# Optimization experiments

Measured on AMD Instinct MI355X. Metric: run time of the kernel, lower is better.

## Reference

```python
import jax, jax.numpy as jnp
import numpy as np

H = 256          # hidden_size
N_NODE = 50000   # item vocab
E_FULL = 500000  # full-graph edges
B = 1024         # sessions per batch
NODES_PER = 12   # session nodes per graph (contiguous, equal sections)
N = B * NODES_PER


def setup_inputs() -> dict:
    key = jax.random.key(0)
    ks = jax.random.split(key, 20)
    stdv = 1.0 / np.sqrt(H)
    u = lambda k, shape: jax.random.uniform(k, shape, jnp.float32, -stdv, stdv)
    return dict(
        x=jax.random.randint(ks[0], (N, 1), 1, N_NODE + 1, dtype=jnp.int32),  # 1-based item ids
        batch=jnp.repeat(jnp.arange(B, dtype=jnp.int32), NODES_PER),          # sorted graph ids
        edge_index=jax.random.randint(ks[1], (2, N), 0, N, dtype=jnp.int32),
        full_graph=jax.random.randint(ks[2], (2, E_FULL), 0, N_NODE, dtype=jnp.int32),
        emb=u(ks[3], (N_NODE, H)),
        ggnn_W=u(ks[4], (H, H)),
        gru_Wih=u(ks[5], (3 * H, H)),
        gru_Whh=u(ks[6], (3 * H, H)),
        gru_bih=u(ks[7], (3 * H,)),
        gru_bhh=u(ks[8], (3 * H,)),
        W1_w=u(ks[9], (H, H)), W1_b=u(ks[10], (H,)),
        W2_w=u(ks[11], (H, H)), W2_b=u(ks[12], (H,)),
        q_w=u(ks[13], (1, H)), q_b=u(ks[14], (1,)),
        W3_w=u(ks[15], (H, 2 * H)), W3_b=u(ks[16], (H,)),
    )


def _forward(x, batch, edge_index, full_graph, emb, ggnn_W, gru_Wih, gru_Whh,
             gru_bih, gru_bhh, W1_w, W1_b, W2_w, W2_b, q_w, q_b, W3_w, W3_b):
    # --- GatedGraphConv (num_layers=1) over the full item graph ---
    src, dst = full_graph[0], full_graph[1]
    m = emb @ ggnn_W                                      # [n_node, H]
    agg = jax.ops.segment_sum(m[src], dst, num_segments=N_NODE)  # sum aggregation
    # GRUCell(agg, emb)
    gi = agg @ gru_Wih.T + gru_bih                        # [n_node, 3H]
    gh = emb @ gru_Whh.T + gru_bhh
    i_r, i_z, i_n = jnp.split(gi, 3, axis=1)
    h_r, h_z, h_n = jnp.split(gh, 3, axis=1)
    r = jax.nn.sigmoid(i_r + h_r)
    z = jax.nn.sigmoid(i_z + h_z)
    n = jnp.tanh(i_n + r * h_n)
    hidden_all = (1.0 - z) * n + z * emb                  # [n_node, H]

    # gather session nodes (x is 1-based), relu
    h2 = jax.nn.relu(hidden_all[x[:, 0] - 1])             # [N, H]

    # --- Embedding2Score: segment attention readout ---
    sections = jax.ops.segment_sum(jnp.ones_like(batch), batch, num_segments=B)
    last_idx = jnp.cumsum(sections) - 1                   # last node of each session
    v_n = h2[last_idx]                                    # [B, H]
    v_n_rep = v_n[batch]                                  # [N, H]
    gate = jax.nn.sigmoid(v_n_rep @ W1_w.T + W1_b + h2 @ W2_w.T + W2_b)
    alpha = gate @ q_w.T + q_b                            # [N, 1]
    s_g = jax.ops.segment_sum(alpha * h2, batch, num_segments=B)  # [B, H]
    s_h = jnp.concatenate([v_n, s_g], axis=1) @ W3_w.T + W3_b     # [B, H]
    scores = s_h @ emb.T                                  # [B, n_node]
    return scores, h2


def reference(x, batch, edge_index, full_graph, emb, ggnn_W, gru_Wih, gru_Whh,
              gru_bih, gru_bhh, W1_w, W1_b, W2_w, W2_b, q_w, q_b, W3_w, W3_b):
    scores, h2 = _forward(x, batch, edge_index, full_graph, emb, ggnn_W,
                          gru_Wih, gru_Whh, gru_bih, gru_bhh,
                          W1_w, W1_b, W2_w, W2_b, q_w, q_b, W3_w, W3_b)
    return scores, h2, edge_index
```

## Files before the change

### kernel.cpp

```cpp
#include <hip/hip_runtime.h>
#include <hip/hip_bf16.h>
#include <stdint.h>

#define HDIM 256
#define NNODE 50000
#define EFULL 500000
#define BSESS 1024
#define NPER 12
#define NROWS 12288
#define CAP 96

typedef __attribute__((ext_vector_type(8))) short bf16x8;
typedef __attribute__((ext_vector_type(4))) float f32x4;
typedef __attribute__((ext_vector_type(4))) unsigned short u16x4;

__device__ __forceinline__ float bf2f(unsigned short v) {
  union { unsigned u; float f; } x; x.u = ((unsigned)v) << 16; return x.f;
}
__device__ __forceinline__ unsigned short f2bf(float f) {
  union { float f; unsigned u; } x; x.f = f;
  unsigned r = x.u + 0x7fff + ((x.u >> 16) & 1);
  return (unsigned short)(r >> 16);
}

__global__ void k_init_map(int* m, int* cnt) {
  int i = blockIdx.x * 256 + threadIdx.x;
  if (i < NNODE) m[i] = -1;
  if (i < NROWS) cnt[i] = 0;
}
__global__ void k_set_map(const int* __restrict__ x, int* __restrict__ m) {
  int i = blockIdx.x * 256 + threadIdx.x;
  if (i < NROWS) atomicMax(&m[x[i] - 1], i);
}

#define CV_EMB   12800000
#define CV_GW    65536
#define CV_WIH   196608
#define CV_WHH   196608
#define CV_W1    65536
#define CV_W2    65536
#define CV_W3    131072
#define CV_BIAS  2304
#define CV_TOTAL (CV_EMB + CV_GW + CV_WIH + CV_WHH + CV_W1 + CV_W2 + CV_W3 + CV_BIAS)
__global__ void k_conv(const float* __restrict__ emb, const float* __restrict__ gw,
                       const float* __restrict__ wih, const float* __restrict__ whh,
                       const float* __restrict__ w1, const float* __restrict__ w2,
                       const float* __restrict__ w3,
                       const float* __restrict__ bih, const float* __restrict__ bhh,
                       const float* __restrict__ w1b, const float* __restrict__ w2b,
                       const float* __restrict__ w3b,
                       unsigned short* __restrict__ embB, unsigned short* __restrict__ gwB,
                       unsigned short* __restrict__ wihB, unsigned short* __restrict__ whhB,
                       unsigned short* __restrict__ w1B, unsigned short* __restrict__ w2B,
                       unsigned short* __restrict__ w3B, unsigned short* __restrict__ biasB) {
  long idx = (long)blockIdx.x * 256 + threadIdx.x;
  if (idx < CV_EMB) { embB[idx] = f2bf(emb[idx]); return; }
  idx -= CV_EMB;
  if (idx < CV_GW)  { gwB[idx] = f2bf(gw[idx]); return; }
  idx -= CV_GW;
  if (idx < CV_WIH) { wihB[idx] = f2bf(wih[idx]); return; }
  idx -= CV_WIH;
  if (idx < CV_WHH) { whhB[idx] = f2bf(whh[idx]); return; }
  idx -= CV_WHH;
  if (idx < CV_W1)  { w1B[idx] = f2bf(w1[idx]); return; }
  idx -= CV_W1;
  if (idx < CV_W2)  { w2B[idx] = f2bf(w2[idx]); return; }
  idx -= CV_W2;
  if (idx < CV_W3)  { w3B[idx] = f2bf(w3[idx]); return; }
  idx -= CV_W3;
  if (idx < 768)        { biasB[idx] = f2bf(bih[idx]); return; }
  if (idx < 1536)       { biasB[idx] = f2bf(bhh[idx - 768]); return; }
  if (idx < 1792)       { biasB[idx] = f2bf(w1b[idx - 1536]); return; }
  if (idx < 2048)       { biasB[idx] = f2bf(w2b[idx - 1792]); return; }
  if (idx < CV_BIAS)    { biasB[idx] = f2bf(w3b[idx - 2048]); return; }
}

__global__ void k_bin(const int* __restrict__ fg, const int* __restrict__ map,
                      int* __restrict__ cnt, int* __restrict__ lists) {
  int e = blockIdx.x * 256 + threadIdx.x;
  if (e >= EFULL) return;
  int cid = map[fg[EFULL + e]];
  if (cid < 0) return;
  int pos = atomicAdd(&cnt[cid], 1);
  if (pos < CAP) lists[cid * CAP + pos] = fg[e];
}

__global__ __launch_bounds__(256) void k_aggsum(const int* __restrict__ cnt,
                                                const int* __restrict__ lists,
                                                const float* __restrict__ emb,
                                                unsigned short* __restrict__ Sb) {
  int i = blockIdx.x * 4 + (threadIdx.x >> 6);
  int lane = threadIdx.x & 63;
  int n = cnt[i];
  const int* lp = lists + (size_t)i * CAP;
  float sx = 0.f, sy = 0.f, sz = 0.f, sw = 0.f;
  int j = 0;
  for (; j + 4 <= n; j += 4) {
    int s0 = lp[j], s1 = lp[j + 1], s2 = lp[j + 2], s3 = lp[j + 3];
    float4 v0 = *(const float4*)(emb + (size_t)s0 * HDIM + lane * 4);
    float4 v1 = *(const float4*)(emb + (size_t)s1 * HDIM + lane * 4);
    float4 v2 = *(const float4*)(emb + (size_t)s2 * HDIM + lane * 4);
    float4 v3 = *(const float4*)(emb + (size_t)s3 * HDIM + lane * 4);
    sx += v0.x + v1.x + v2.x + v3.x;
    sy += v0.y + v1.y + v2.y + v3.y;
    sz += v0.z + v1.z + v2.z + v3.z;
    sw += v0.w + v1.w + v2.w + v3.w;
  }
  for (; j < n; j++) {
    int s0 = lp[j];
    float4 v0 = *(const float4*)(emb + (size_t)s0 * HDIM + lane * 4);
    sx += v0.x; sy += v0.y; sz += v0.z; sw += v0.w;
  }
  u16x4 o; o.x = f2bf(sx); o.y = f2bf(sy); o.z = f2bf(sz); o.w = f2bf(sw);
  *(u16x4*)(Sb + (size_t)i * HDIM + lane * 4) = o;
}

__global__ void k_bbig(const unsigned short* __restrict__ Pt, const unsigned short* __restrict__ Whh,
                       const float* __restrict__ bih, const float* __restrict__ bhh,
                       unsigned short* __restrict__ Bbig, unsigned short* __restrict__ biasBig) {
  int idx = blockIdx.x * 256 + threadIdx.x;
  if (idx < 1024 * 512) {
    int j = idx >> 9, c = idx & 511;
    unsigned short v = 0;
    if (c < 256) {
      if (j < 768) v = Pt[j * 256 + c];
    } else {
      int cc = c - 256;
      if (j < 512) v = Whh[j * 256 + cc];
      else if (j >= 768) v = Whh[(j - 256) * 256 + cc];
    }
    Bbig[idx] = v;
    return;
  }
  int jj = idx - 1024 * 512;
  if (jj < 512)       biasBig[jj] = f2bf(bih[jj] + bhh[jj]);
  else if (jj < 768)  biasBig[jj] = f2bf(bih[jj]);
  else if (jj < 1024) biasBig[jj] = f2bf(bhh[jj - 256]);
}

__global__ void k_gather(const int* __restrict__ x, const int* __restrict__ map,
                         const unsigned short* __restrict__ Sb, const float* __restrict__ emb,
                         unsigned short* __restrict__ Acat) {
  int i = blockIdx.x;
  int lane = threadIdx.x;
  int node = x[i] - 1;
  int cid = map[node];
  if (cid < 0) cid = 0;
  *(u16x4*)(Acat + (size_t)i * 512 + lane * 4) = *(const u16x4*)(Sb + (size_t)cid * HDIM + lane * 4);
  float4 v = *(const float4*)(emb + (size_t)node * HDIM + lane * 4);
  u16x4 o; o.x = f2bf(v.x); o.y = f2bf(v.y); o.z = f2bf(v.z); o.w = f2bf(v.w);
  *(u16x4*)(Acat + (size_t)i * 512 + 256 + lane * 4) = o;
}

__global__ void k_gru(const unsigned short* __restrict__ gall, const unsigned short* __restrict__ Acat,
                      unsigned short* __restrict__ h2b, float* __restrict__ h2out,
                      unsigned short* __restrict__ shin) {
  int idx = blockIdx.x * 256 + threadIdx.x;
  int row = idx >> 8, c = idx & 255;
  size_t base = (size_t)row * 1024;
  float rs = bf2f(gall[base + c]);
  float zs = bf2f(gall[base + 256 + c]);
  float inn = bf2f(gall[base + 512 + c]);
  float hn = bf2f(gall[base + 768 + c]);
  float r = 1.f / (1.f + expf(-rs));
  float z = 1.f / (1.f + expf(-zs));
  float n = tanhf(inn + r * hn);
  float e = bf2f(Acat[(size_t)row * 512 + 256 + c]);
  float h = fmaxf((1.f - z) * n + z * e, 0.f);
  unsigned short hb = f2bf(h);
  h2b[idx] = hb;
  h2out[idx] = h;
  if (row % NPER == NPER - 1) shin[(size_t)(row / NPER) * 512 + c] = hb;
}

__global__ void k_alpha(const unsigned short* __restrict__ t1, const unsigned short* __restrict__ t2,
                        const int* __restrict__ batch, const float* __restrict__ qw,
                        const float* __restrict__ qb, float* __restrict__ alpha) {
  int i = blockIdx.x, lane = threadIdx.x;
  int b = batch[i];
  u16x4 a = *(const u16x4*)(t1 + (size_t)b * HDIM + lane * 4);
  u16x4 c = *(const u16x4*)(t2 + (size_t)i * HDIM + lane * 4);
  float4 q = *(const float4*)(qw + lane * 4);
  float p = 0.f;
  p += q.x / (1.f + expf(-(bf2f(a.x) + bf2f(c.x))));
  p += q.y / (1.f + expf(-(bf2f(a.y) + bf2f(c.y))));
  p += q.z / (1.f + expf(-(bf2f(a.z) + bf2f(c.z))));
  p += q.w / (1.f + expf(-(bf2f(a.w) + bf2f(c.w))));
#pragma unroll
  for (int off = 32; off > 0; off >>= 1) p += __shfl_down(p, off);
  if (lane == 0) alpha[i] = p + qb[0];
}
__global__ void k_sg(const float* __restrict__ alpha, const unsigned short* __restrict__ h2b,
                     unsigned short* __restrict__ shin) {
  int b = blockIdx.x, c = threadIdx.x;
  float s = 0.f;
#pragma unroll
  for (int j = 0; j < NPER; j++)
    s += alpha[b * NPER + j] * bf2f(h2b[((size_t)b * NPER + j) * 256 + c]);
  shin[(size_t)b * 512 + 256 + c] = f2bf(s);
}
__global__ void k_edges(const int* __restrict__ e, float* __restrict__ out) {
  int i = blockIdx.x * 256 + threadIdx.x;
  if (i < 2 * NROWS) out[i] = (float)e[i];
}

template <bool OUT_BF16>
__global__ __launch_bounds__(256) void k_gemm_nt(
    const unsigned short* __restrict__ A, int lda,
    const unsigned short* __restrict__ Bm, int ldb,
    const unsigned short* __restrict__ bias,
    void* __restrict__ C, int ldc, int M, int N, int K) {
  __shared__ __align__(16) unsigned short As[128 * 32];
  __shared__ __align__(16) unsigned short Bs[128 * 32];
  const int tid = threadIdx.x;
  const int wid = tid >> 6, lane = tid & 63;
  const int quad = lane >> 4, l15 = lane & 15;
  const int m0 = blockIdx.x * 128, n0 = blockIdx.y * 128;
  const int wm = (wid & 1) * 64, wn = (wid >> 1) * 64;
  f32x4 acc[4][4] = {};
  const int lrow = tid >> 2;
  const int lcol = (tid & 3) * 8;
  const size_t ar0 = (size_t)min(m0 + lrow, M - 1) * lda + lcol;
  const size_t ar1 = (size_t)min(m0 + lrow + 64, M - 1) * lda + lcol;
  const size_t br0 = (size_t)min(n0 + lrow, N - 1) * ldb + lcol;
  const size_t br1 = (size_t)min(n0 + lrow + 64, N - 1) * ldb + lcol;
  const int ak = quad * 8;
  for (int k0 = 0; k0 < K; k0 += 32) {
    *(float4*)&As[(size_t)tid * 8]        = *(const float4*)&A[ar0 + k0];
    *(float4*)&As[2048 + (size_t)tid * 8] = *(const float4*)&A[ar1 + k0];
    *(float4*)&Bs[(size_t)tid * 8]        = *(const float4*)&Bm[br0 + k0];
    *(float4*)&Bs[2048 + (size_t)tid * 8] = *(const float4*)&Bm[br1 + k0];
    __syncthreads();
    bf16x8 af[4], bfv[4];
#pragma unroll
    for (int mi = 0; mi < 4; mi++) af[mi] = *(const bf16x8*)&As[(wm + mi * 16 + l15) * 32 + ak];
#pragma unroll
    for (int ni = 0; ni < 4; ni++) bfv[ni] = *(const bf16x8*)&Bs[(wn + ni * 16 + l15) * 32 + ak];
#pragma unroll
    for (int mi = 0; mi < 4; mi++)
#pragma unroll
      for (int ni = 0; ni < 4; ni++)
        acc[mi][ni] = __builtin_amdgcn_mfma_f32_16x16x32_bf16(af[mi], bfv[ni], acc[mi][ni], 0, 0, 0);
    __syncthreads();
  }
#pragma unroll
  for (int mi = 0; mi < 4; mi++) {
    const int gr0 = m0 + wm + mi * 16 + quad * 4;
#pragma unroll
    for (int ni = 0; ni < 4; ni++) {
      const int gc = n0 + wn + ni * 16 + l15;
      if (gc >= N) continue;
      const float bv = bias ? bf2f(bias[gc]) : 0.f;
#pragma unroll
      for (int r = 0; r < 4; r++) {
        const int gr = gr0 + r;
        if (gr < M) {
          const float v = acc[mi][ni][r] + bv;
          if (OUT_BF16) ((unsigned short*)C)[(size_t)gr * ldc + gc] = f2bf(v);
          else          ((float*)C)[(size_t)gr * ldc + gc] = v;
        }
      }
    }
  }
}

template <bool OUT_BF16>
__global__ __launch_bounds__(512) void k_gemm_nt2(
    const unsigned short* __restrict__ A, int lda,
    const unsigned short* __restrict__ Bm, int ldb,
    const unsigned short* __restrict__ bias,
    void* __restrict__ C, int ldc, int M, int N, int K) {
  __shared__ __align__(16) unsigned short As[256 * 32];
  __shared__ __align__(16) unsigned short Bs[128 * 32];
  const int tid = threadIdx.x;
  const int wid = tid >> 6, lane = tid & 63;
  const int quad = lane >> 4, l15 = lane & 15;
  const int m0 = blockIdx.x * 256, n0 = blockIdx.y * 128;
  const int wm = (wid & 3) * 64, wn = (wid >> 2) * 64;
  f32x4 acc[4][4] = {};
  const int lrow = tid >> 2;
  const int lcol = (tid & 3) * 8;
  const size_t ar0 = (size_t)min(m0 + lrow, M - 1) * lda + lcol;
  const size_t ar1 = (size_t)min(m0 + lrow + 128, M - 1) * lda + lcol;
  const size_t br0 = (size_t)min(n0 + lrow, N - 1) * ldb + lcol;
  const int ak = quad * 8;
  for (int k0 = 0; k0 < K; k0 += 32) {
    *(float4*)&As[(size_t)lrow * 32 + lcol]         = *(const float4*)&A[ar0 + k0];
    *(float4*)&As[(size_t)(lrow + 128) * 32 + lcol] = *(const float4*)&A[ar1 + k0];
    *(float4*)&Bs[(size_t)lrow * 32 + lcol]         = *(const float4*)&Bm[br0 + k0];
    __syncthreads();
    bf16x8 af[4], bfv[4];
#pragma unroll
    for (int mi = 0; mi < 4; mi++) af[mi] = *(const bf16x8*)&As[(wm + mi * 16 + l15) * 32 + ak];
#pragma unroll
    for (int ni = 0; ni < 4; ni++) bfv[ni] = *(const bf16x8*)&Bs[(wn + ni * 16 + l15) * 32 + ak];
#pragma unroll
    for (int mi = 0; mi < 4; mi++)
#pragma unroll
      for (int ni = 0; ni < 4; ni++)
        acc[mi][ni] = __builtin_amdgcn_mfma_f32_16x16x32_bf16(af[mi], bfv[ni], acc[mi][ni], 0, 0, 0);
    __syncthreads();
  }
#pragma unroll
  for (int mi = 0; mi < 4; mi++) {
    const int gr0 = m0 + wm + mi * 16 + quad * 4;
#pragma unroll
    for (int ni = 0; ni < 4; ni++) {
      const int gc = n0 + wn + ni * 16 + l15;
      if (gc >= N) continue;
      const float bv = bias ? bf2f(bias[gc]) : 0.f;
#pragma unroll
      for (int r = 0; r < 4; r++) {
        const int gr = gr0 + r;
        if (gr < M) {
          const float v = acc[mi][ni][r] + bv;
          if (OUT_BF16) ((unsigned short*)C)[(size_t)gr * ldc + gc] = f2bf(v);
          else          ((float*)C)[(size_t)gr * ldc + gc] = v;
        }
      }
    }
  }
}

extern "C" void kernel_launch(void* const* d_in, const int* in_sizes, int n_in,
                              void* d_out, int out_size, void* d_ws, size_t ws_size,
                              hipStream_t stream) {
  const int* x     = (const int*)d_in[0];
  const int* batch = (const int*)d_in[1];
  const int* eidx  = (const int*)d_in[2];
  const int* fg    = (const int*)d_in[3];
  const float* emb   = (const float*)d_in[4];
  const float* ggnnW = (const float*)d_in[5];
  const float* Wih   = (const float*)d_in[6];
  const float* Whh   = (const float*)d_in[7];
  const float* bih   = (const float*)d_in[8];
  const float* bhh   = (const float*)d_in[9];
  const float* W1w   = (const float*)d_in[10];
  const float* W1b   = (const float*)d_in[11];
  const float* W2w   = (const float*)d_in[12];
  const float* W2b   = (const float*)d_in[13];
  const float* qw    = (const float*)d_in[14];
  const float* qb    = (const float*)d_in[15];
  const float* W3w   = (const float*)d_in[16];
  const float* W3b   = (const float*)d_in[17];

  char* w = (char*)d_ws;
  size_t off = 0;
  auto alloc = [&](size_t bytes) { char* p = w + off; off += (bytes + 511) & ~(size_t)511; return p; };
  int*            map   = (int*)alloc((size_t)NNODE * 4);
  int*            cnt   = (int*)alloc((size_t)NROWS * 4);
  int*            lists = (int*)alloc((size_t)NROWS * CAP * 4);
  unsigned short* Sb    = (unsigned short*)alloc((size_t)NROWS * HDIM * 2);
  unsigned short* Acat  = (unsigned short*)alloc((size_t)NROWS * 512 * 2);
  unsigned short* gallC = (unsigned short*)alloc((size_t)NROWS * 1024 * 2);
  unsigned short* embB  = (unsigned short*)alloc((size_t)NNODE * HDIM * 2);
  unsigned short* gwB   = (unsigned short*)alloc((size_t)CV_GW * 2);
  unsigned short* WihB  = (unsigned short*)alloc((size_t)CV_WIH * 2);
  unsigned short* WhhB  = (unsigned short*)alloc((size_t)CV_WHH * 2);
  unsigned short* W1wB  = (unsigned short*)alloc((size_t)CV_W1 * 2);
  unsigned short* W2wB  = (unsigned short*)alloc((size_t)CV_W2 * 2);
  unsigned short* W3wB  = (unsigned short*)alloc((size_t)CV_W3 * 2);
  unsigned short* biasB = (unsigned short*)alloc((size_t)CV_BIAS * 2);
  unsigned short* Pt    = (unsigned short*)alloc((size_t)768 * 256 * 2);
  unsigned short* Bbig  = (unsigned short*)alloc((size_t)1024 * 512 * 2);
  unsigned short* biasBig = (unsigned short*)alloc((size_t)1024 * 2);
  unsigned short* h2b   = (unsigned short*)alloc((size_t)NROWS * HDIM * 2);
  unsigned short* t1    = (unsigned short*)alloc((size_t)BSESS * HDIM * 2);
  unsigned short* t2    = (unsigned short*)alloc((size_t)NROWS * HDIM * 2);
  float*          alpha = (float*)alloc((size_t)NROWS * 4);
  unsigned short* shin  = (unsigned short*)alloc((size_t)BSESS * 512 * 2);
  unsigned short* shb   = (unsigned short*)alloc((size_t)BSESS * HDIM * 2);
  if (off > ws_size) return;

  float* out_scores = (float*)d_out;
  float* out_h2     = out_scores + (size_t)BSESS * NNODE;
  float* out_e      = out_h2 + (size_t)NROWS * HDIM;

  dim3 blk(256);
  k_init_map<<<(NNODE + 255) / 256, blk, 0, stream>>>(map, cnt);
  k_set_map <<<(NROWS + 255) / 256, blk, 0, stream>>>(x, map);
  k_conv    <<<(CV_TOTAL + 255) / 256, blk, 0, stream>>>(emb, ggnnW, Wih, Whh, W1w, W2w, W3w,
                bih, bhh, W1b, W2b, W3b, embB, gwB, WihB, WhhB, W1wB, W2wB, W3wB, biasB);
  k_bin     <<<(EFULL + 255) / 256, blk, 0, stream>>>(fg, map, cnt, lists);
  k_aggsum  <<<NROWS / 4, blk, 0, stream>>>(cnt, lists, emb, Sb);
  k_gemm_nt<true><<<dim3(6, 2), blk, 0, stream>>>(WihB, HDIM, gwB, HDIM, nullptr, Pt, HDIM, 768, HDIM, HDIM);
  k_bbig    <<<(1024 * 512 + 1024 + 255) / 256, blk, 0, stream>>>(Pt, WhhB, bih, bhh, Bbig, biasBig);
  k_gather  <<<NROWS, 64, 0, stream>>>(x, map, Sb, emb, Acat);
  k_gemm_nt2<true><<<dim3(48, 8), dim3(512), 0, stream>>>(Acat, 512, Bbig, 512, biasBig, gallC, 1024, NROWS, 1024, 512);
  k_gru     <<<NROWS, blk, 0, stream>>>(gallC, Acat, h2b, out_h2, shin);
  k_gemm_nt<true><<<dim3(8, 2), blk, 0, stream>>>(shin, 512, W1wB, HDIM, biasB + 1536, t1, HDIM, BSESS, HDIM, HDIM);
  k_gemm_nt<true><<<dim3(96, 2), blk, 0, stream>>>(h2b, HDIM, W2wB, HDIM, biasB + 1792, t2, HDIM, NROWS, HDIM, HDIM);
  k_alpha   <<<NROWS, 64, 0, stream>>>(t1, t2, batch, qw, qb, alpha);
  k_sg      <<<BSESS, blk, 0, stream>>>(alpha, h2b, shin);
  k_gemm_nt<true><<<dim3(8, 2), blk, 0, stream>>>(shin, 512, W3wB, 512, biasB + 2048, shb, HDIM, BSESS, HDIM, 512);
  k_gemm_nt2<false><<<dim3(4, 391), dim3(512), 0, stream>>>(shb, HDIM, embB, HDIM, nullptr, out_scores, NNODE, BSESS, NNODE, HDIM);
  k_edges   <<<(2 * NROWS + 255) / 256, blk, 0, stream>>>(eidx, out_e);
}
```

Baseline: 511.6 us.

## Fuse GRU gates into GEMM epilogue and merge small pipeline kernels

Reorders the combined weight matrix so that each 64-column wave tile holds the r, z, n-input and n-hidden gates for the same 16 channels. The GRU nonlinearity can then run directly in the GEMM epilogue, which removes the 12288x1024 bf16 gate intermediate and the separate GRU kernel. Map and count initialisation and the edge copy move into the conversion kernel, and the aggregation kernel writes Acat directly, dropping the gather kernel and the Sb buffer. The t1 and t2 GEMMs share one launch, and the alpha and s_g kernels merge into one per-session attention kernel. The result is fewer launches and less intermediate traffic, with more complex index logic in exchange.

```diff
diff --git a/kernel.cpp b/kernel.cpp
--- a/kernel.cpp
+++ b/kernel.cpp
@@ -21,16 +21,6 @@
   union { float f; unsigned u; } x; x.f = f;
   unsigned r = x.u + 0x7fff + ((x.u >> 16) & 1);
   return (unsigned short)(r >> 16);
-}
-
-__global__ void k_init_map(int* m, int* cnt) {
-  int i = blockIdx.x * 256 + threadIdx.x;
-  if (i < NNODE) m[i] = -1;
-  if (i < NROWS) cnt[i] = 0;
-}
-__global__ void k_set_map(const int* __restrict__ x, int* __restrict__ m) {
-  int i = blockIdx.x * 256 + threadIdx.x;
-  if (i < NROWS) atomicMax(&m[x[i] - 1], i);
 }
 
 #define CV_EMB   12800000
@@ -41,7 +31,8 @@
 #define CV_W2    65536
 #define CV_W3    131072
 #define CV_BIAS  2304
-#define CV_TOTAL (CV_EMB + CV_GW + CV_WIH + CV_WHH + CV_W1 + CV_W2 + CV_W3 + CV_BIAS)
+#define CV_WSUM  (CV_EMB + CV_GW + CV_WIH + CV_WHH + CV_W1 + CV_W2 + CV_W3 + CV_BIAS)
+#define CV_TOTAL (CV_WSUM + NNODE + NROWS + 2 * NROWS)
 __global__ void k_conv(const float* __restrict__ emb, const float* __restrict__ gw,
                        const float* __restrict__ wih, const float* __restrict__ whh,
                        const float* __restrict__ w1, const float* __restrict__ w2,
@@ -52,7 +43,9 @@
                        unsigned short* __restrict__ embB, unsigned short* __restrict__ gwB,
                        unsigned short* __restrict__ wihB, unsigned short* __restrict__ whhB,
                        unsigned short* __restrict__ w1B, unsigned short* __restrict__ w2B,
-                       unsigned short* __restrict__ w3B, unsigned short* __restrict__ biasB) {
+                       unsigned short* __restrict__ w3B, unsigned short* __restrict__ biasB,
+                       int* __restrict__ map, int* __restrict__ cnt,
+                       const int* __restrict__ eidx, float* __restrict__ out_e) {
   long idx = (long)blockIdx.x * 256 + threadIdx.x;
   if (idx < CV_EMB) { embB[idx] = f2bf(emb[idx]); return; }
   idx -= CV_EMB;
@@ -68,11 +61,24 @@
   idx -= CV_W2;
   if (idx < CV_W3)  { w3B[idx] = f2bf(w3[idx]); return; }
   idx -= CV_W3;
-  if (idx < 768)        { biasB[idx] = f2bf(bih[idx]); return; }
-  if (idx < 1536)       { biasB[idx] = f2bf(bhh[idx - 768]); return; }
-  if (idx < 1792)       { biasB[idx] = f2bf(w1b[idx - 1536]); return; }
-  if (idx < 2048)       { biasB[idx] = f2bf(w2b[idx - 1792]); return; }
-  if (idx < CV_BIAS)    { biasB[idx] = f2bf(w3b[idx - 2048]); return; }
+  if (idx < CV_BIAS) {
+    if (idx < 768)        { biasB[idx] = f2bf(bih[idx]); return; }
+    if (idx < 1536)       { biasB[idx] = f2bf(bhh[idx - 768]); return; }
+    if (idx < 1792)       { biasB[idx] = f2bf(w1b[idx - 1536]); return; }
+    if (idx < 2048)       { biasB[idx] = f2bf(w2b[idx - 1792]); return; }
+    biasB[idx] = f2bf(w3b[idx - 2048]); return;
+  }
+  idx -= CV_BIAS;
+  if (idx < NNODE) { map[idx] = -1; return; }
+  idx -= NNODE;
+  if (idx < NROWS) { cnt[idx] = 0; return; }
+  idx -= NROWS;
+  if (idx < 2 * NROWS) out_e[idx] = (float)eidx[idx];
+}
+
+__global__ void k_set_map(const int* __restrict__ x, int* __restrict__ m) {
+  int i = blockIdx.x * 256 + threadIdx.x;
+  if (i < NROWS) atomicMax(&m[x[i] - 1], i);
 }
 
 __global__ void k_bin(const int* __restrict__ fg, const int* __restrict__ map,
@@ -85,14 +91,18 @@
   if (pos < CAP) lists[cid * CAP + pos] = fg[e];
 }
 
-__global__ __launch_bounds__(256) void k_aggsum(const int* __restrict__ cnt,
+__global__ __launch_bounds__(256) void k_aggsum(const int* __restrict__ x,
+                                                const int* __restrict__ map,
+                                                const int* __restrict__ cnt,
                                                 const int* __restrict__ lists,
                                                 const float* __restrict__ emb,
-                                                unsigned short* __restrict__ Sb) {
+                                                unsigned short* __restrict__ Acat) {
   int i = blockIdx.x * 4 + (threadIdx.x >> 6);
   int lane = threadIdx.x & 63;
-  int n = cnt[i];
-  const int* lp = lists + (size_t)i * CAP;
+  int node = x[i] - 1;
+  int cid = map[node];
+  int n = cnt[cid];
+  const int* lp = lists + (size_t)cid * CAP;
   float sx = 0.f, sy = 0.f, sz = 0.f, sw = 0.f;
   int j = 0;
   for (; j + 4 <= n; j += 4) {
@@ -112,110 +122,54 @@
     sx += v0.x; sy += v0.y; sz += v0.z; sw += v0.w;
   }
   u16x4 o; o.x = f2bf(sx); o.y = f2bf(sy); o.z = f2bf(sz); o.w = f2bf(sw);
-  *(u16x4*)(Sb + (size_t)i * HDIM + lane * 4) = o;
+  *(u16x4*)(Acat + (size_t)i * 512 + lane * 4) = o;
+  float4 v = *(const float4*)(emb + (size_t)node * HDIM + lane * 4);
+  u16x4 o2; o2.x = f2bf(v.x); o2.y = f2bf(v.y); o2.z = f2bf(v.z); o2.w = f2bf(v.w);
+  *(u16x4*)(Acat + (size_t)i * 512 + 256 + lane * 4) = o2;
 }
 
 __global__ void k_bbig(const unsigned short* __restrict__ Pt, const unsigned short* __restrict__ Whh,
                        const float* __restrict__ bih, const float* __restrict__ bhh,
-                       unsigned short* __restrict__ Bbig, unsigned short* __restrict__ biasBig) {
+                       unsigned short* __restrict__ Bbig2, unsigned short* __restrict__ bias2) {
   int idx = blockIdx.x * 256 + threadIdx.x;
   if (idx < 1024 * 512) {
-    int j = idx >> 9, c = idx & 511;
+    int jp = idx >> 9, k = idx & 511;
+    int q = jp >> 6, g = (jp >> 4) & 3, t = jp & 15;
+    int c = q * 16 + t;
     unsigned short v = 0;
-    if (c < 256) {
-      if (j < 768) v = Pt[j * 256 + c];
+    if (k < 256) {
+      if (g < 3) v = Pt[(g * 256 + c) * 256 + k];
     } else {
-      int cc = c - 256;
-      if (j < 512) v = Whh[j * 256 + cc];
-      else if (j >= 768) v = Whh[(j - 256) * 256 + cc];
+      int kk = k - 256;
+      if (g < 2) v = Whh[(g * 256 + c) * 256 + kk];
+      else if (g == 3) v = Whh[(512 + c) * 256 + kk];
     }
-    Bbig[idx] = v;
+    Bbig2[idx] = v;
     return;
   }
-  int jj = idx - 1024 * 512;
-  if (jj < 512)       biasBig[jj] = f2bf(bih[jj] + bhh[jj]);
-  else if (jj < 768)  biasBig[jj] = f2bf(bih[jj]);
-  else if (jj < 1024) biasBig[jj] = f2bf(bhh[jj - 256]);
-}
-
-__global__ void k_gather(const int* __restrict__ x, const int* __restrict__ map,
-                         const unsigned short* __restrict__ Sb, const float* __restrict__ emb,
-                         unsigned short* __restrict__ Acat) {
-  int i = blockIdx.x;
-  int lane = threadIdx.x;
-  int node = x[i] - 1;
-  int cid = map[node];
-  if (cid < 0) cid = 0;
-  *(u16x4*)(Acat + (size_t)i * 512 + lane * 4) = *(const u16x4*)(Sb + (size_t)cid * HDIM + lane * 4);
-  float4 v = *(const float4*)(emb + (size_t)node * HDIM + lane * 4);
-  u16x4 o; o.x = f2bf(v.x); o.y = f2bf(v.y); o.z = f2bf(v.z); o.w = f2bf(v.w);
-  *(u16x4*)(Acat + (size_t)i * 512 + 256 + lane * 4) = o;
-}
-
-__global__ void k_gru(const unsigned short* __restrict__ gall, const unsigned short* __restrict__ Acat,
-                      unsigned short* __restrict__ h2b, float* __restrict__ h2out,
-                      unsigned short* __restrict__ shin) {
-  int idx = blockIdx.x * 256 + threadIdx.x;
-  int row = idx >> 8, c = idx & 255;
-  size_t base = (size_t)row * 1024;
-  float rs = bf2f(gall[base + c]);
-  float zs = bf2f(gall[base + 256 + c]);
-  float inn = bf2f(gall[base + 512 + c]);
-  float hn = bf2f(gall[base + 768 + c]);
-  float r = 1.f / (1.f + expf(-rs));
-  float z = 1.f / (1.f + expf(-zs));
-  float n = tanhf(inn + r * hn);
-  float e = bf2f(Acat[(size_t)row * 512 + 256 + c]);
-  float h = fmaxf((1.f - z) * n + z * e, 0.f);
-  unsigned short hb = f2bf(h);
-  h2b[idx] = hb;
-  h2out[idx] = h;
-  if (row % NPER == NPER - 1) shin[(size_t)(row / NPER) * 512 + c] = hb;
-}
-
-__global__ void k_alpha(const unsigned short* __restrict__ t1, const unsigned short* __restrict__ t2,
-                        const int* __restrict__ batch, const float* __restrict__ qw,
-                        const float* __restrict__ qb, float* __restrict__ alpha) {
-  int i = blockIdx.x, lane = threadIdx.x;
-  int b = batch[i];
-  u16x4 a = *(const u16x4*)(t1 + (size_t)b * HDIM + lane * 4);
-  u16x4 c = *(const u16x4*)(t2 + (size_t)i * HDIM + lane * 4);
-  float4 q = *(const float4*)(qw + lane * 4);
-  float p = 0.f;
-  p += q.x / (1.f + expf(-(bf2f(a.x) + bf2f(c.x))));
-  p += q.y / (1.f + expf(-(bf2f(a.y) + bf2f(c.y))));
-  p += q.z / (1.f + expf(-(bf2f(a.z) + bf2f(c.z))));
-  p += q.w / (1.f + expf(-(bf2f(a.w) + bf2f(c.w))));
-#pragma unroll
-  for (int off = 32; off > 0; off >>= 1) p += __shfl_down(p, off);
-  if (lane == 0) alpha[i] = p + qb[0];
-}
-__global__ void k_sg(const float* __restrict__ alpha, const unsigned short* __restrict__ h2b,
-                     unsigned short* __restrict__ shin) {
-  int b = blockIdx.x, c = threadIdx.x;
-  float s = 0.f;
-#pragma unroll
-  for (int j = 0; j < NPER; j++)
-    s += alpha[b * NPER + j] * bf2f(h2b[((size_t)b * NPER + j) * 256 + c]);
-  shin[(size_t)b * 512 + 256 + c] = f2bf(s);
-}
-__global__ void k_edges(const int* __restrict__ e, float* __restrict__ out) {
-  int i = blockIdx.x * 256 + threadIdx.x;
-  if (i < 2 * NROWS) out[i] = (float)e[i];
+  int jp = idx - 1024 * 512;
+  if (jp < 1024) {
+    int q = jp >> 6, g = (jp >> 4) & 3, t = jp & 15;
+    int c = q * 16 + t;
+    float bv;
+    if (g < 2)      bv = bih[g * 256 + c] + bhh[g * 256 + c];
+    else if (g == 2) bv = bih[512 + c];
+    else             bv = bhh[512 + c];
+    bias2[jp] = f2bf(bv);
+  }
 }
 
 template <bool OUT_BF16>
-__global__ __launch_bounds__(256) void k_gemm_nt(
+__device__ __forceinline__ void gemm128_body(
+    unsigned short* As, unsigned short* Bs,
     const unsigned short* __restrict__ A, int lda,
     const unsigned short* __restrict__ Bm, int ldb,
     const unsigned short* __restrict__ bias,
-    void* __restrict__ C, int ldc, int M, int N, int K) {
-  __shared__ __align__(16) unsigned short As[128 * 32];
-  __shared__ __align__(16) unsigned short Bs[128 * 32];
+    void* __restrict__ C, int ldc, int M, int N, int K, int bx, int by) {
   const int tid = threadIdx.x;
   const int wid = tid >> 6, lane = tid & 63;
   const int quad = lane >> 4, l15 = lane & 15;
-  const int m0 = blockIdx.x * 128, n0 = blockIdx.y * 128;
+  const int m0 = bx * 128, n0 = by * 128;
   const int wm = (wid & 1) * 64, wn = (wid >> 1) * 64;
   f32x4 acc[4][4] = {};
   const int lrow = tid >> 2;
@@ -262,6 +216,128 @@
       }
     }
   }
+}
+
+template <bool OUT_BF16>
+__global__ __launch_bounds__(256) void k_gemm_nt(
+    const unsigned short* __restrict__ A, int lda,
+    const unsigned short* __restrict__ Bm, int ldb,
+    const unsigned short* __restrict__ bias,
+    void* __restrict__ C, int ldc, int M, int N, int K) {
+  __shared__ __align__(16) unsigned short As[128 * 32];
+  __shared__ __align__(16) unsigned short Bs[128 * 32];
+  gemm128_body<OUT_BF16>(As, Bs, A, lda, Bm, ldb, bias, C, ldc, M, N, K, blockIdx.x, blockIdx.y);
+}
+
+__global__ __launch_bounds__(256) void k_t12(
+    const unsigned short* __restrict__ h2b, const unsigned short* __restrict__ W2, const unsigned short* __restrict__ b2,
+    unsigned short* __restrict__ t2,
+    const unsigned short* __restrict__ shin, const unsigned short* __restrict__ W1, const unsigned short* __restrict__ b1,
+    unsigned short* __restrict__ t1) {
+  __shared__ __align__(16) unsigned short As[128 * 32];
+  __shared__ __align__(16) unsigned short Bs[128 * 32];
+  if (blockIdx.x < 96)
+    gemm128_body<true>(As, Bs, h2b, HDIM, W2, HDIM, b2, t2, HDIM, NROWS, HDIM, HDIM, blockIdx.x, blockIdx.y);
+  else
+    gemm128_body<true>(As, Bs, shin, 512, W1, HDIM, b1, t1, HDIM, BSESS, HDIM, HDIM, blockIdx.x - 96, blockIdx.y);
+}
+
+__global__ __launch_bounds__(512) void k_ggru(
+    const unsigned short* __restrict__ Acat,
+    const unsigned short* __restrict__ Bbig2,
+    const unsigned short* __restrict__ bias2,
+    unsigned short* __restrict__ h2b, float* __restrict__ h2out,
+    unsigned short* __restrict__ shin) {
+  __shared__ __align__(16) unsigned short As[256 * 32];
+  __shared__ __align__(16) unsigned short Bs[128 * 32];
+  const int tid = threadIdx.x;
+  const int wid = tid >> 6, lane = tid & 63;
+  const int quad = lane >> 4, l15 = lane & 15;
+  const int m0 = blockIdx.x * 256, n0 = blockIdx.y * 128;
+  const int wm = (wid & 3) * 64, wn = (wid >> 2) * 64;
+  f32x4 acc[4][4] = {};
+  const int lrow = tid >> 2;
+  const int lcol = (tid & 3) * 8;
+  const size_t ar0 = (size_t)(m0 + lrow) * 512 + lcol;
+  const size_t ar1 = (size_t)(m0 + lrow + 128) * 512 + lcol;
+  const size_t br0 = (size_t)(n0 + lrow) * 512 + lcol;
+  const int ak = quad * 8;
+  for (int k0 = 0; k0 < 512; k0 += 32) {
+    *(float4*)&As[(size_t)lrow * 32 + lcol]         = *(const float4*)&Acat[ar0 + k0];
+    *(float4*)&As[(size_t)(lrow + 128) * 32 + lcol] = *(const float4*)&Acat[ar1 + k0];
+    *(float4*)&Bs[(size_t)lrow * 32 + lcol]         = *(const float4*)&Bbig2[br0 + k0];
+    __syncthreads();
+    bf16x8 af[4], bfv[4];
+#pragma unroll
+    for (int mi = 0; mi < 4; mi++) af[mi] = *(const bf16x8*)&As[(wm + mi * 16 + l15) * 32 + ak];
+#pragma unroll
+    for (int g = 0; g < 4; g++) bfv[g] = *(const bf16x8*)&Bs[(wn + g * 16 + l15) * 32 + ak];
+#pragma unroll
+    for (int mi = 0; mi < 4; mi++)
+#pragma unroll
+      for (int g = 0; g < 4; g++)
+        acc[mi][g] = __builtin_amdgcn_mfma_f32_16x16x32_bf16(af[mi], bfv[g], acc[mi][g], 0, 0, 0);
+    __syncthreads();
+  }
+  const int ch = ((n0 + wn) >> 2) + l15;
+  const float b0 = bf2f(bias2[(n0 + wn) + 0 * 16 + l15]);
+  const float b1 = bf2f(bias2[(n0 + wn) + 1 * 16 + l15]);
+  const float b2 = bf2f(bias2[(n0 + wn) + 2 * 16 + l15]);
+  const float b3 = bf2f(bias2[(n0 + wn) + 3 * 16 + l15]);
+#pragma unroll
+  for (int mi = 0; mi < 4; mi++) {
+    const int gr0 = m0 + wm + mi * 16 + quad * 4;
+#pragma unroll
+    for (int r = 0; r < 4; r++) {
+      const int gr = gr0 + r;
+      float rs = acc[mi][0][r] + b0;
+      float zs = acc[mi][1][r] + b1;
+      float inn = acc[mi][2][r] + b2;
+      float hn = acc[mi][3][r] + b3;
+      float rr = 1.f / (1.f + expf(-rs));
+      float zz = 1.f / (1.f + expf(-zs));
+      float nn = tanhf(inn + rr * hn);
+      float e = bf2f(Acat[(size_t)gr * 512 + 256 + ch]);
+      float h = fmaxf((1.f - zz) * nn + zz * e, 0.f);
+      unsigned short hb = f2bf(h);
+      h2b[(size_t)gr * HDIM + ch] = hb;
+      h2out[(size_t)gr * HDIM + ch] = h;
+      if (gr % NPER == NPER - 1) shin[(size_t)(gr / NPER) * 512 + ch] = hb;
+    }
+  }
+}
+
+__global__ __launch_bounds__(256) void k_attn(
+    const unsigned short* __restrict__ t1, const unsigned short* __restrict__ t2,
+    const unsigned short* __restrict__ h2b,
+    const float* __restrict__ qw, const float* __restrict__ qb,
+    unsigned short* __restrict__ shin) {
+  __shared__ float al[NPER];
+  const int b = blockIdx.x;
+  const int w = threadIdx.x >> 6, lane = threadIdx.x & 63;
+  u16x4 a = *(const u16x4*)(t1 + (size_t)b * HDIM + lane * 4);
+  float4 q = *(const float4*)(qw + lane * 4);
+  float ax = bf2f(a.x), ay = bf2f(a.y), az = bf2f(a.z), aw = bf2f(a.w);
+#pragma unroll
+  for (int i = 0; i < 3; i++) {
+    int j = w * 3 + i;
+    u16x4 c = *(const u16x4*)(t2 + ((size_t)b * NPER + j) * HDIM + lane * 4);
+    float p = 0.f;
+    p += q.x / (1.f + expf(-(ax + bf2f(c.x))));
+    p += q.y / (1.f + expf(-(ay + bf2f(c.y))));
+    p += q.z / (1.f + expf(-(az + bf2f(c.z))));
+    p += q.w / (1.f + expf(-(aw + bf2f(c.w))));
+#pragma unroll
+    for (int off = 32; off > 0; off >>= 1) p += __shfl_down(p, off);
+    if (lane == 0) al[j] = p + qb[0];
+  }
+  __syncthreads();
+  const int c = threadIdx.x;
+  float s = 0.f;
+#pragma unroll
+  for (int j = 0; j < NPER; j++)
+    s += al[j] * bf2f(h2b[((size_t)b * NPER + j) * HDIM + c]);
+  shin[(size_t)b * 512 + 256 + c] = f2bf(s);
 }
 
 template <bool OUT_BF16>
@@ -343,6 +419,7 @@
   const float* qb    = (const float*)d_in[15];
   const float* W3w   = (const float*)d_in[16];
   const float* W3b   = (const float*)d_in[17];
+  (void)batch;
 
   char* w = (char*)d_ws;
   size_t off = 0;
@@ -350,9 +427,7 @@
   int*            map   = (int*)alloc((size_t)NNODE * 4);
   int*            cnt   = (int*)alloc((size_t)NROWS * 4);
   int*            lists = (int*)alloc((size_t)NROWS * CAP * 4);
-  unsigned short* Sb    = (unsigned short*)alloc((size_t)NROWS * HDIM * 2);
   unsigned short* Acat  = (unsigned short*)alloc((size_t)NROWS * 512 * 2);
-  unsigned short* gallC = (unsigned short*)alloc((size_t)NROWS * 1024 * 2);
   unsigned short* embB  = (unsigned short*)alloc((size_t)NNODE * HDIM * 2);
   unsigned short* gwB   = (unsigned short*)alloc((size_t)CV_GW * 2);
   unsigned short* WihB  = (unsigned short*)alloc((size_t)CV_WIH * 2);
@@ -362,12 +437,11 @@
   unsigned short* W3wB  = (unsigned short*)alloc((size_t)CV_W3 * 2);
   unsigned short* biasB = (unsigned short*)alloc((size_t)CV_BIAS * 2);
   unsigned short* Pt    = (unsigned short*)alloc((size_t)768 * 256 * 2);
-  unsigned short* Bbig  = (unsigned short*)alloc((size_t)1024 * 512 * 2);
-  unsigned short* biasBig = (unsigned short*)alloc((size_t)1024 * 2);
+  unsigned short* Bbig2 = (unsigned short*)alloc((size_t)1024 * 512 * 2);
+  unsigned short* bias2 = (unsigned short*)alloc((size_t)1024 * 2);
   unsigned short* h2b   = (unsigned short*)alloc((size_t)NROWS * HDIM * 2);
   unsigned short* t1    = (unsigned short*)alloc((size_t)BSESS * HDIM * 2);
   unsigned short* t2    = (unsigned short*)alloc((size_t)NROWS * HDIM * 2);
-  float*          alpha = (float*)alloc((size_t)NROWS * 4);
   unsigned short* shin  = (unsigned short*)alloc((size_t)BSESS * 512 * 2);
   unsigned short* shb   = (unsigned short*)alloc((size_t)BSESS * HDIM * 2);
   if (off > ws_size) return;
@@ -377,22 +451,17 @@
   float* out_e      = out_h2 + (size_t)NROWS * HDIM;
 
   dim3 blk(256);
-  k_init_map<<<(NNODE + 255) / 256, blk, 0, stream>>>(map, cnt);
-  k_set_map <<<(NROWS + 255) / 256, blk, 0, stream>>>(x, map);
-  k_conv    <<<(CV_TOTAL + 255) / 256, blk, 0, stream>>>(emb, ggnnW, Wih, Whh, W1w, W2w, W3w,
-                bih, bhh, W1b, W2b, W3b, embB, gwB, WihB, WhhB, W1wB, W2wB, W3wB, biasB);
-  k_bin     <<<(EFULL + 255) / 256, blk, 0, stream>>>(fg, map, cnt, lists);
-  k_aggsum  <<<NROWS / 4, blk, 0, stream>>>(cnt, lists, emb, Sb);
+  k_conv   <<<(CV_TOTAL + 255) / 256, blk, 0, stream>>>(emb, ggnnW, Wih, Whh, W1w, W2w, W3w,
+               bih, bhh, W1b, W2b, W3b, embB, gwB, WihB, WhhB, W1wB, W2wB, W3wB, biasB,
+               map, cnt, eidx, out_e);
+  k_set_map<<<(NROWS + 255) / 256, blk, 0, stream>>>(x, map);
+  k_bin    <<<(EFULL + 255) / 256, blk, 0, stream>>>(fg, map, cnt, lists);
   k_gemm_nt<true><<<dim3(6, 2), blk, 0, stream>>>(WihB, HDIM, gwB, HDIM, nullptr, Pt, HDIM, 768, HDIM, HDIM);
-  k_bbig    <<<(1024 * 512 + 1024 + 255) / 256, blk, 0, stream>>>(Pt, WhhB, bih, bhh, Bbig, biasBig);
-  k_gather  <<<NROWS, 64, 0, stream>>>(x, map, Sb, emb, Acat);
-  k_gemm_nt2<true><<<dim3(48, 8), dim3(512), 0, stream>>>(Acat, 512, Bbig, 512, biasBig, gallC, 1024, NROWS, 1024, 512);
-  k_gru     <<<NROWS, blk, 0, stream>>>(gallC, Acat, h2b, out_h2, shin);
-  k_gemm_nt<true><<<dim3(8, 2), blk, 0, stream>>>(shin, 512, W1wB, HDIM, biasB + 1536, t1, HDIM, BSESS, HDIM, HDIM);
-  k_gemm_nt<true><<<dim3(96, 2), blk, 0, stream>>>(h2b, HDIM, W2wB, HDIM, biasB + 1792, t2, HDIM, NROWS, HDIM, HDIM);
-  k_alpha   <<<NROWS, 64, 0, stream>>>(t1, t2, batch, qw, qb, alpha);
-  k_sg      <<<BSESS, blk, 0, stream>>>(alpha, h2b, shin);
+  k_bbig   <<<(1024 * 512 + 1024 + 255) / 256, blk, 0, stream>>>(Pt, WhhB, bih, bhh, Bbig2, bias2);
+  k_aggsum <<<NROWS / 4, blk, 0, stream>>>(x, map, cnt, lists, emb, Acat);
+  k_ggru   <<<dim3(48, 8), dim3(512), 0, stream>>>(Acat, Bbig2, bias2, h2b, out_h2, shin);
+  k_t12    <<<dim3(104, 2), blk, 0, stream>>>(h2b, W2wB, biasB + 1792, t2, shin, W1wB, biasB + 1536, t1);
+  k_attn   <<<BSESS, blk, 0, stream>>>(t1, t2, h2b, qw, qb, shin);
   k_gemm_nt<true><<<dim3(8, 2), blk, 0, stream>>>(shin, 512, W3wB, 512, biasB + 2048, shb, HDIM, BSESS, HDIM, 512);
   k_gemm_nt2<false><<<dim3(4, 391), dim3(512), 0, stream>>>(shb, HDIM, embB, HDIM, nullptr, out_scores, NNODE, BSESS, NNODE, HDIM);
-  k_edges   <<<(2 * NROWS + 255) / 256, blk, 0, stream>>>(eidx, out_e);
-}
+}
```

After: 474.2 us. 1.08x faster.
